# Kernel tuning notes

Measured on AMD Instinct MI355X. Metric: run time of the kernel, lower is better.

The kernel has to match this reference:

```python
import jax, jax.numpy as jnp
import numpy as np
import math

NUM_HEADS = 16
GRID_SIZE = 32
NUM_BUCKETS = 32
MAX_DISTANCE = 128
EMBED_DIM = 1024


def _rel_pos_bucket(rel, num_buckets, max_distance):
    # T5-style bucketing, as written in the source (int truncation of log branch)
    is_neg = (rel < 0).astype(jnp.int32)
    rel = jnp.abs(rel)
    rel = jnp.clip(rel, 0, max_distance - 1)
    max_exact = num_buckets // 2
    log_branch = max_exact + (
        jnp.log(rel.astype(jnp.float32) / max_exact)
        / math.log(max_distance / max_exact)
        * (num_buckets - max_exact)
    ).astype(jnp.int32)
    bucket = is_neg * num_buckets + jnp.where(rel < max_exact, rel.astype(jnp.int32), log_branch)
    return bucket  # in [0, 2*num_buckets)


def setup_inputs() -> dict:
    key = jax.random.key(0)
    ks = jax.random.split(key, 9)
    B, N, D = 4, GRID_SIZE * GRID_SIZE, EMBED_DIM
    s = 0.02
    return {
        "query": jax.random.normal(ks[0], (B, N, D), jnp.float32),
        "key": jax.random.normal(ks[1], (B, N, D), jnp.float32),
        "value": jax.random.normal(ks[2], (B, N, D), jnp.float32),
        "in_proj_w": jax.random.normal(ks[3], (3 * D, D), jnp.float32) * s,
        "in_proj_b": jnp.zeros((3 * D,), jnp.float32),
        "out_proj_w": jax.random.normal(ks[4], (D, D), jnp.float32) * s,
        "out_proj_b": jnp.zeros((D,), jnp.float32),
        "rel_bias_table": jax.random.normal(ks[5], (2 * NUM_BUCKETS, NUM_HEADS), jnp.float32) * s,
    }


def reference(query, key, value, in_proj_w, in_proj_b, out_proj_w, out_proj_b, rel_bias_table):
    B, N, D = query.shape
    H = NUM_HEADS
    hd = D // H
    scaling = hd ** -0.5

    # in_proj applied to `query` only (source ignores key/value args)
    qkv = query @ in_proj_w.T + in_proj_b          # [B, N, 3D]
    q, k, v = jnp.split(qkv, 3, axis=-1)
    q = q.reshape(B, N, H, hd).transpose(0, 2, 1, 3)  # [B, H, N, hd]
    k = k.reshape(B, N, H, hd).transpose(0, 2, 1, 3)
    v = v.reshape(B, N, H, hd).transpose(0, 2, 1, 3)

    attn = jnp.einsum("bhnd,bhmd->bhnm", q, k) * scaling  # [B, H, N, N]

    # 2D relative-position bucket bias
    idx = jnp.arange(N)
    row = idx // GRID_SIZE
    col = idx % GRID_SIZE
    row_bucket = _rel_pos_bucket(row[:, None] - row[None, :], NUM_BUCKETS, MAX_DISTANCE)
    col_bucket = _rel_pos_bucket(col[:, None] - col[None, :], NUM_BUCKETS, MAX_DISTANCE)
    bias = rel_bias_table[row_bucket] + rel_bias_table[col_bucket]  # [N, N, H]
    attn = attn + bias.transpose(2, 0, 1)[None]  # [B, H, N, N]

    attn_weights = jax.nn.softmax(attn, axis=-1)
    out = jnp.einsum("bhnm,bhmd->bhnd", attn_weights, v)  # [B, H, N, hd]
    out = out.transpose(0, 2, 1, 3).reshape(B, N, D)
    out = out @ out_proj_w.T + out_proj_b
    return out, attn_weights
```

## Files before the change

### kernel.cpp

```cpp
#include <hip/hip_runtime.h>
#include <hip/hip_bf16.h>

typedef __attribute__((ext_vector_type(8))) short bf16x8;
typedef __attribute__((ext_vector_type(4))) float f32x4;
typedef __attribute__((ext_vector_type(4))) unsigned short us4;

#define MFMA16(a,b,c) __builtin_amdgcn_mfma_f32_16x16x32_bf16((a),(b),(c),0,0,0)

__device__ __forceinline__ unsigned short f2bf(float f){
  unsigned u = __builtin_bit_cast(unsigned, f);
  u += 0x7fffu + ((u>>16)&1u);
  return (unsigned short)(u>>16);
}
__device__ __forceinline__ float bf2f(unsigned short h){
  unsigned u = ((unsigned)h)<<16;
  return __builtin_bit_cast(float, u);
}
__device__ __forceinline__ void gload_lds16(const unsigned short* g, unsigned short* l){
  __builtin_amdgcn_global_load_lds((const __attribute__((address_space(1))) void*)g,
                                   (__attribute__((address_space(3))) void*)l,
                                   16, 0, 0);
}

__global__ __launch_bounds__(256) void cast_all(
    const float* __restrict__ q, const float* __restrict__ wi, const float* __restrict__ wo,
    unsigned short* __restrict__ qq, unsigned short* __restrict__ wib, unsigned short* __restrict__ wob)
{
  int i4 = (blockIdx.x*256 + threadIdx.x)*4;
  const float* src; unsigned short* dst; int off;
  if (i4 < 4194304)       { src=q;  dst=qq;  off=i4; }
  else if (i4 < 7340032)  { src=wi; dst=wib; off=i4-4194304; }
  else                    { src=wo; dst=wob; off=i4-7340032; }
  float4 v = *(const float4*)(src+off);
  us4 o; o.x=f2bf(v.x); o.y=f2bf(v.y); o.z=f2bf(v.z); o.w=f2bf(v.w);
  *(us4*)(dst+off) = o;
}

__global__ __launch_bounds__(256) void gemm_qkv(
    const unsigned short* __restrict__ A, const unsigned short* __restrict__ Bw,
    const float* __restrict__ bias,
    unsigned short* __restrict__ qo, unsigned short* __restrict__ ko, unsigned short* __restrict__ vTo)
{
  __shared__ unsigned short lA[128*64];
  __shared__ unsigned short lB[128*64];
  int tid = threadIdx.x, lane = tid&63, w = tid>>6;
  int wr = (w>>1)<<6, wc = (w&1)<<6;
  int lin = blockIdx.y*24 + blockIdx.x;
  int xcd = lin & 7, idx = lin >> 3;
  int rg = xcd >> 1, cg = xcd & 1;
  int rowT = ((rg<<3) + (idx & 7)) << 7;
  int colT = (cg*12 + (idx >> 3)) << 7;
  f32x4 acc[4][4] = {};
  for (int k0=0; k0<1024; k0+=64){
    #pragma unroll
    for (int it=0; it<4; ++it){
      int ci = it*256+tid; int r=ci>>3, cs=ci&7;
      int c = (cs ^ (r&7))<<3;
      gload_lds16(A + (size_t)(rowT+r)*1024 + k0 + c, &lA[ci<<3]);
    }
    #pragma unroll
    for (int it=0; it<4; ++it){
      int ci = it*256+tid; int r=ci>>3, cs=ci&7;
      int c = (cs ^ (r&7))<<3;
      gload_lds16(Bw + (size_t)(colT+r)*1024 + k0 + c, &lB[ci<<3]);
    }
    asm volatile("s_waitcnt vmcnt(0)" ::: "memory");
    __syncthreads();
    #pragma unroll
    for (int kk=0; kk<2; ++kk){
      int kc = (kk<<2) + (lane>>4);
      bf16x8 a[4], b[4];
      #pragma unroll
      for (int i=0;i<4;++i){
        int r = wr + (i<<4) + (lane&15);
        a[i] = *(const bf16x8*)&lA[(r<<6) + ((kc ^ (r&7))<<3)];
      }
      #pragma unroll
      for (int j=0;j<4;++j){
        int r = wc + (j<<4) + (lane&15);
        b[j] = *(const bf16x8*)&lB[(r<<6) + ((kc ^ (r&7))<<3)];
      }
      #pragma unroll
      for (int i=0;i<4;++i)
        #pragma unroll
        for (int j=0;j<4;++j)
          acc[i][j] = MFMA16(a[i], b[j], acc[i][j]);
    }
    __syncthreads();
  }
  int sec = colT >> 10;
  #pragma unroll
  for (int i=0;i<4;++i){
    #pragma unroll
    for (int j=0;j<4;++j){
      int cg2 = colT + wc + (j<<4) + (lane&15);
      int d = cg2 & 1023, hh = d>>6, di = d&63;
      float bsv = bias[cg2];
      #pragma unroll
      for (int q=0;q<4;++q){
        int m = rowT + wr + (i<<4) + ((lane>>4)<<2) + q;
        int b = m>>10, n = m&1023;
        unsigned short bv = f2bf(acc[i][j][q] + bsv);
        size_t bh = (size_t)((b<<4) + hh);
        if (sec==0)      qo[(bh<<16) + ((size_t)n<<6) + di] = bv;
        else if (sec==1) ko[(bh<<16) + ((size_t)n<<6) + di] = bv;
        else             vTo[(bh<<16) + ((size_t)di<<10) + n] = bv;
      }
    }
  }
}

__global__ __launch_bounds__(512) void gemm_out(
    const unsigned short* __restrict__ A, const unsigned short* __restrict__ Bw,
    const float* __restrict__ bias, float* __restrict__ out)
{
  __shared__ unsigned short lA[128*64];
  __shared__ unsigned short lB[128*64];
  int tid = threadIdx.x, lane = tid&63, w = tid>>6;
  int wr = (w>>2)<<6;
  int wc = (w&3)<<5;
  int lin = blockIdx.y*8 + blockIdx.x;
  int xcd = lin & 7, idx = lin >> 3;
  int rg = xcd >> 1, cg = xcd & 1;
  int rowT = ((rg<<3) + (idx & 7)) << 7;
  int colT = ((cg<<2) + (idx >> 3)) << 7;
  f32x4 acc[4][2] = {};
  for (int k0=0; k0<1024; k0+=64){
    #pragma unroll
    for (int it=0; it<2; ++it){
      int ci = it*512+tid; int r=ci>>3, cs=ci&7;
      int c = (cs ^ (r&7))<<3;
      gload_lds16(A + (size_t)(rowT+r)*1024 + k0 + c, &lA[ci<<3]);
      gload_lds16(Bw + (size_t)(colT+r)*1024 + k0 + c, &lB[ci<<3]);
    }
    asm volatile("s_waitcnt vmcnt(0)" ::: "memory");
    __syncthreads();
    #pragma unroll
    for (int kk=0; kk<2; ++kk){
      int kc = (kk<<2) + (lane>>4);
      bf16x8 a[4], b[2];
      #pragma unroll
      for (int i=0;i<4;++i){
        int r = wr + (i<<4) + (lane&15);
        a[i] = *(const bf16x8*)&lA[(r<<6) + ((kc ^ (r&7))<<3)];
      }
      #pragma unroll
      for (int j=0;j<2;++j){
        int r = wc + (j<<4) + (lane&15);
        b[j] = *(const bf16x8*)&lB[(r<<6) + ((kc ^ (r&7))<<3)];
      }
      #pragma unroll
      for (int i=0;i<4;++i)
        #pragma unroll
        for (int j=0;j<2;++j)
          acc[i][j] = MFMA16(a[i], b[j], acc[i][j]);
    }
    __syncthreads();
  }
  #pragma unroll
  for (int i=0;i<4;++i){
    #pragma unroll
    for (int j=0;j<2;++j){
      int cg2 = colT + wc + (j<<4) + (lane&15);
      float bsv = bias[cg2];
      #pragma unroll
      for (int q=0;q<4;++q){
        int m = rowT + wr + (i<<4) + ((lane>>4)<<2) + q;
        out[(size_t)m*1024 + cg2] = acc[i][j][q] + bsv;
      }
    }
  }
}

__global__ __launch_bounds__(256) void attn_fused(
    const unsigned short* __restrict__ qbf, const unsigned short* __restrict__ kbf,
    const unsigned short* __restrict__ vT, const float* __restrict__ tbl,
    float* __restrict__ attn_out, unsigned short* __restrict__ oa)
{
  __shared__ unsigned short P[32*1024];
  __shared__ unsigned short qs[32*64];
  __shared__ float biasv[64];
  __shared__ float rsum[4][32];
  __shared__ float rinv_s[32];

  int tid=threadIdx.x, lane=tid&63, w=tid>>6;
  int bid = blockIdx.x;
  int wgid = ((bid&7)<<8) + (bid>>3);
  int pair = wgid >> 5;
  int stripe = wgid & 31;
  int h = pair & 15;
  int bg = pair >> 4;
  int nbase = stripe<<5;
  const unsigned short* qg = qbf + ((size_t)pair<<16) + ((size_t)nbase<<6);
  const unsigned short* kg = kbf + ((size_t)pair<<16);
  const unsigned short* vg = vT  + ((size_t)pair<<16);

  if (tid < 63){
    int dd = tid - 31;
    int neg = dd<0 ? 1:0;
    int a = dd<0 ? -dd : dd;
    int bkt;
    if (a<16) bkt = a;
    else bkt = 16 + (int)(__logf((float)a*(1.f/16.f)) * (16.f/__logf(8.f)));
    bkt += neg*32;
    biasv[tid] = tbl[(bkt<<4) + h];
  }
  { int r=tid>>3, cs=tid&7;
    int c = (cs ^ (r&7))<<3;
    gload_lds16(qg + (r<<6) + c, &qs[tid<<3]); }
  asm volatile("s_waitcnt vmcnt(0)" ::: "memory");
  __syncthreads();

  int x = lane&15, g = lane>>4;
  float cterm[3][4];
  #pragma unroll
  for (int s=0;s<3;++s)
    #pragma unroll
    for (int q=0;q<4;++q)
      cterm[s][q] = biasv[(g<<2) + q - x + 31 + ((s-1)<<4)];

  bf16x8 qa[2][2];
  #pragma unroll
  for (int rt=0;rt<2;++rt){
    int r = (rt<<4) + x;
    #pragma unroll
    for (int hh=0;hh<2;++hh)
      qa[rt][hh] = *(const bf16x8*)&qs[(r<<6) + ((((hh<<2)+g) ^ (r&7))<<3)];
  }

  float rs[2][4] = {};
  int colW = w<<8;
  const unsigned short* kbase = kg + ((size_t)x<<6) + (g<<3);
  bf16x8 nb0 = *(const bf16x8*)(kbase + ((size_t)colW<<6));
  bf16x8 nb1 = *(const bf16x8*)(kbase + ((size_t)colW<<6) + 32);
  #pragma unroll 2
  for (int t=0; t<16; ++t){
    bf16x8 bk0 = nb0, bk1 = nb1;
    if (t < 15){
      const unsigned short* kp = kbase + ((size_t)(colW + ((t+1)<<4))<<6);
      nb0 = *(const bf16x8*)kp;
      nb1 = *(const bf16x8*)(kp+32);
    }
    int cb = colW + (t<<4);
    int j = cb + x;
    int par = t&1;
    float rterm = biasv[stripe - (cb>>5) + 31];
    #pragma unroll
    for (int rt=0; rt<2; ++rt){
      f32x4 acc = {};
      acc = MFMA16(qa[rt][0], bk0, acc);
      acc = MFMA16(qa[rt][1], bk1, acc);
      #pragma unroll
      for (int q=0;q<4;++q){
        int r = (rt<<4) + (g<<2) + q;
        float lg = acc[q]*0.125f + rterm + cterm[rt+1-par][q];
        float e = __expf(lg);
        rs[rt][q] += e;
        int byteoff = (r<<11) + ((((j>>3) ^ (r&7)))<<4) + ((j&7)<<1);
        *(unsigned short*)((char*)P + byteoff) = f2bf(e);
      }
    }
  }
  #pragma unroll
  for (int rt=0;rt<2;++rt){
    #pragma unroll
    for (int q=0;q<4;++q){
      float v = rs[rt][q];
      v += __shfl_xor(v,1); v += __shfl_xor(v,2); v += __shfl_xor(v,4); v += __shfl_xor(v,8);
      if (x==0) rsum[w][(rt<<4)+(g<<2)+q] = v;
    }
  }
  __syncthreads();
  if (tid<32) rinv_s[tid] = 1.f/(rsum[0][tid]+rsum[1][tid]+rsum[2][tid]+rsum[3][tid]);
  __syncthreads();

  float* ao = attn_out + ((size_t)pair<<20) + ((size_t)nbase<<10);
  f32x4 oacc[2] = {};
  int dbase = w<<4;
  const unsigned short* vp = vg + ((size_t)(dbase + x)<<10) + (g<<3);
  for (int cbk=0; cbk<8; ++cbk){
    #pragma unroll
    for (int it=0; it<2; ++it){
      int r = (it<<4) + (tid>>4);
      int c8 = (cbk<<7) + ((tid&15)<<3);
      int byteoff = (r<<11) + ((((c8>>3) ^ (r&7)))<<4);
      bf16x8 pv8 = *(const bf16x8*)((char*)P + byteoff);
      float ri = rinv_s[r];
      float4 o0, o1;
      o0.x = bf2f((unsigned short)pv8[0])*ri;
      o0.y = bf2f((unsigned short)pv8[1])*ri;
      o0.z = bf2f((unsigned short)pv8[2])*ri;
      o0.w = bf2f((unsigned short)pv8[3])*ri;
      o1.x = bf2f((unsigned short)pv8[4])*ri;
      o1.y = bf2f((unsigned short)pv8[5])*ri;
      o1.z = bf2f((unsigned short)pv8[6])*ri;
      o1.w = bf2f((unsigned short)pv8[7])*ri;
      *(float4*)(ao + ((size_t)r<<10) + c8)     = o0;
      *(float4*)(ao + ((size_t)r<<10) + c8 + 4) = o1;
    }
    #pragma unroll
    for (int ks=0; ks<4; ++ks){
      int kc = (cbk<<7) + (ks<<5);
      bf16x8 bv = *(const bf16x8*)(vp + kc);
      int ck = (kc>>3) + g;
      #pragma unroll
      for (int rt=0;rt<2;++rt){
        int r = (rt<<4) + x;
        bf16x8 a = *(const bf16x8*)((char*)P + (r<<11) + ((ck ^ (r&7))<<4));
        oacc[rt] = MFMA16(a, bv, oacc[rt]);
      }
    }
  }
  #pragma unroll
  for (int rt=0;rt<2;++rt){
    #pragma unroll
    for (int q=0;q<4;++q){
      int r = (rt<<4) + (g<<2) + q;
      float val = oacc[rt][q]*rinv_s[r];
      oa[((size_t)((bg<<10) + nbase + r)<<10) + (h<<6) + dbase + x] = f2bf(val);
    }
  }
}

extern "C" void kernel_launch(void* const* d_in, const int* in_sizes, int n_in,
                              void* d_out, int out_size, void* d_ws, size_t ws_size,
                              hipStream_t stream)
{
  const float* query = (const float*)d_in[0];
  const float* wi  = (const float*)d_in[3];
  const float* bi  = (const float*)d_in[4];
  const float* wo  = (const float*)d_in[5];
  const float* bo  = (const float*)d_in[6];
  const float* tbl = (const float*)d_in[7];

  char* ws = (char*)d_ws;
  unsigned short* qq  = (unsigned short*)(ws);
  unsigned short* wib = (unsigned short*)(ws + 8388608);
  unsigned short* wob = (unsigned short*)(ws + 14680064);
  unsigned short* qbf = (unsigned short*)(ws + 16777216);
  unsigned short* kbf = (unsigned short*)(ws + 25165824);
  unsigned short* vTb = (unsigned short*)(ws + 33554432);
  unsigned short* oa  = (unsigned short*)(ws + 41943040);

  float* out  = (float*)d_out;
  float* attn = out + 4194304;

  cast_all<<<dim3(8192), dim3(256), 0, stream>>>(query, wi, wo, qq, wib, wob);
  gemm_qkv<<<dim3(24,32), dim3(256), 0, stream>>>(qq, wib, bi, qbf, kbf, vTb);
  attn_fused<<<dim3(2048), dim3(256), 0, stream>>>(qbf, kbf, vTb, tbl, attn, oa);
  gemm_out<<<dim3(8,32), dim3(512), 0, stream>>>(oa, wob, bo, out);
}
```

Measured before the change: 176.2 us.

## Double-buffer LDS tiles in QKV GEMM with K-step 32 prefetch

The QKV projection GEMM now splits LDS into two buffers of 128x32 tiles and issues the global-to-LDS loads for the next K-slice before running the MFMAs on the current one. This overlaps memory latency with compute instead of waiting for each 64-wide K tile before computing, and it halves the per-iteration tile size and adjusts the XOR swizzle to match. In exchange there are twice as many loop iterations and barriers, and each iteration does less MFMA work to hide the load latency.

Result: no change. 178.3 us (+1.2%).

```diff
diff --git a/kernel.cpp b/kernel.cpp
--- a/kernel.cpp
+++ b/kernel.cpp
@@ -41,8 +41,8 @@
     const float* __restrict__ bias,
     unsigned short* __restrict__ qo, unsigned short* __restrict__ ko, unsigned short* __restrict__ vTo)
 {
-  __shared__ unsigned short lA[128*64];
-  __shared__ unsigned short lB[128*64];
+  __shared__ unsigned short lA[2][128*32];
+  __shared__ unsigned short lB[2][128*32];
   int tid = threadIdx.x, lane = tid&63, w = tid>>6;
   int wr = (w>>1)<<6, wc = (w&1)<<6;
   int lin = blockIdx.y*24 + blockIdx.x;
@@ -50,44 +50,52 @@
   int rg = xcd >> 1, cg = xcd & 1;
   int rowT = ((rg<<3) + (idx & 7)) << 7;
   int colT = (cg*12 + (idx >> 3)) << 7;
+  int x = lane&15, g = lane>>4;
   f32x4 acc[4][4] = {};
-  for (int k0=0; k0<1024; k0+=64){
-    #pragma unroll
-    for (int it=0; it<4; ++it){
-      int ci = it*256+tid; int r=ci>>3, cs=ci&7;
-      int c = (cs ^ (r&7))<<3;
-      gload_lds16(A + (size_t)(rowT+r)*1024 + k0 + c, &lA[ci<<3]);
-    }
-    #pragma unroll
-    for (int it=0; it<4; ++it){
-      int ci = it*256+tid; int r=ci>>3, cs=ci&7;
-      int c = (cs ^ (r&7))<<3;
-      gload_lds16(Bw + (size_t)(colT+r)*1024 + k0 + c, &lB[ci<<3]);
-    }
+
+  #pragma unroll
+  for (int it=0; it<2; ++it){
+    int ci = it*256+tid; int r=ci>>2, cs=ci&3;
+    int c = (cs ^ ((r>>1)&3))<<3;
+    gload_lds16(A  + (size_t)(rowT+r)*1024 + c, &lA[0][ci<<3]);
+    gload_lds16(Bw + (size_t)(colT+r)*1024 + c, &lB[0][ci<<3]);
+  }
+  asm volatile("s_waitcnt vmcnt(0)" ::: "memory");
+  __syncthreads();
+
+  #pragma unroll 2
+  for (int t=0; t<32; ++t){
+    int buf = t&1, nb = buf^1;
+    if (t < 31){
+      int k1 = (t+1)<<5;
+      #pragma unroll
+      for (int it=0; it<2; ++it){
+        int ci = it*256+tid; int r=ci>>2, cs=ci&3;
+        int c = (cs ^ ((r>>1)&3))<<3;
+        gload_lds16(A  + (size_t)(rowT+r)*1024 + k1 + c, &lA[nb][ci<<3]);
+        gload_lds16(Bw + (size_t)(colT+r)*1024 + k1 + c, &lB[nb][ci<<3]);
+      }
+    }
+    bf16x8 a[4], b[4];
+    #pragma unroll
+    for (int i=0;i<4;++i){
+      int r = wr + (i<<4) + x;
+      a[i] = *(const bf16x8*)&lA[buf][(r<<5) + ((g ^ ((r>>1)&3))<<3)];
+    }
+    #pragma unroll
+    for (int j=0;j<4;++j){
+      int r = wc + (j<<4) + x;
+      b[j] = *(const bf16x8*)&lB[buf][(r<<5) + ((g ^ ((r>>1)&3))<<3)];
+    }
+    #pragma unroll
+    for (int i=0;i<4;++i)
+      #pragma unroll
+      for (int j=0;j<4;++j)
+        acc[i][j] = MFMA16(a[i], b[j], acc[i][j]);
     asm volatile("s_waitcnt vmcnt(0)" ::: "memory");
     __syncthreads();
-    #pragma unroll
-    for (int kk=0; kk<2; ++kk){
-      int kc = (kk<<2) + (lane>>4);
-      bf16x8 a[4], b[4];
-      #pragma unroll
-      for (int i=0;i<4;++i){
-        int r = wr + (i<<4) + (lane&15);
-        a[i] = *(const bf16x8*)&lA[(r<<6) + ((kc ^ (r&7))<<3)];
-      }
-      #pragma unroll
-      for (int j=0;j<4;++j){
-        int r = wc + (j<<4) + (lane&15);
-        b[j] = *(const bf16x8*)&lB[(r<<6) + ((kc ^ (r&7))<<3)];
-      }
-      #pragma unroll
-      for (int i=0;i<4;++i)
-        #pragma unroll
-        for (int j=0;j<4;++j)
-          acc[i][j] = MFMA16(a[i], b[j], acc[i][j]);
-    }
-    __syncthreads();
-  }
+  }
+
   int sec = colT >> 10;
   #pragma unroll
   for (int i=0;i<4;++i){
```
